# Kernel tuning notes

Hardware: AMD Instinct MI355X
Metric: run time of the kernel (lower is better)

Reference implementation:

```python
import jax, jax.numpy as jnp
import numpy as np

T = 4096
INPUT_SIZE = 64
DIMS = 64          # __init__ forces dimensions = input_size
RESERVOIR = 2048
OUTPUT_SIZE = 1
SPECTRAL_RADIUS = 0.95


def setup_inputs() -> dict:
    key = jax.random.key(0)
    k_x, k_c, k_in, k_res, k_w, k_b = jax.random.split(key, 6)
    X = jax.random.normal(k_x, (T, INPUT_SIZE, 1), dtype=jnp.float32)
    # conversion matrix: random then QR -> orthonormal columns
    C_raw = jax.random.uniform(k_c, (DIMS, INPUT_SIZE), dtype=jnp.float32)
    C, _ = jnp.linalg.qr(C_raw)
    # ESN weights. W_res entries ~ N(0, 1/RESERVOIR): circular-law spectral
    # radius ~= 1, scaled to the target spectral radius.
    W_in = jax.random.uniform(k_in, (RESERVOIR, DIMS), dtype=jnp.float32, minval=-1.0, maxval=1.0)
    W_res = jax.random.normal(k_res, (RESERVOIR, RESERVOIR), dtype=jnp.float32) * (SPECTRAL_RADIUS / np.sqrt(RESERVOIR))
    dense_W = jax.random.normal(k_w, (OUTPUT_SIZE, RESERVOIR + DIMS), dtype=jnp.float32) * 0.02
    dense_b = jnp.zeros((OUTPUT_SIZE,), dtype=jnp.float32)
    return {"X": X, "C": C, "W_in": W_in, "W_res": W_res,
            "dense_W": dense_W, "dense_b": dense_b}


def reference(X, C, W_in, W_res, dense_W, dense_b):
    # project all inputs up front: u_t = C @ x_t   -> (T, DIMS)
    U = jnp.einsum('di,tio->tdo', C, X)[..., 0]
    # sequential reservoir recurrence: h_t = tanh(W_in u_t + W_res h_{t-1})
    def step(h, u):
        h_new = jnp.tanh(W_in @ u + W_res @ h)
        return h_new, h_new
    h0 = jnp.zeros((W_res.shape[0],), dtype=X.dtype)
    _, H = jax.lax.scan(step, h0, U)            # (T, RESERVOIR)
    # ESN forward returns vstack(u, h); dense1 reads its transpose
    feats = jnp.concatenate([U, H], axis=1)     # (T, DIMS + RESERVOIR)
    y = feats @ dense_W.T + dense_b             # (T, OUTPUT_SIZE)
    # torch: stack of (1, OUTPUT) rows -> (T,1,OUT), permute(0,2,1) -> (T,OUT,1)
    return y[:, :, None]
```

## Files before the change

### kernel.cpp

```cpp
#include <hip/hip_runtime.h>

#define TT 4096

typedef __attribute__((ext_vector_type(2))) unsigned int u2v;
typedef __attribute__((ext_vector_type(4))) unsigned int u4v;
typedef __attribute__((ext_vector_type(2))) __fp16 f16x2;
typedef __attribute__((ext_vector_type(2))) _Float16 F16x2;
union HU { unsigned int u; f16x2 hf; F16x2 hF; };


__global__ void esn_prep(const float* __restrict__ C,
                         const float* __restrict__ Win,
                         const float* __restrict__ dW,
                         float* __restrict__ M,
                         float* __restrict__ wtil) {
  __shared__ float s[64];
  const int b = blockIdx.x, i = threadIdx.x;
  if (b < 2048) {
    s[i] = Win[b * 64 + i];
    __syncthreads();
    float acc = 0.f;
#pragma unroll 16
    for (int d = 0; d < 64; ++d) acc += s[d] * C[d * 64 + i];
    M[b * 64 + i] = acc;
  } else {
    s[i] = dW[i];
    __syncthreads();
    float acc = 0.f;
    for (int d = 0; d < 64; ++d) acc += s[d] * C[d * 64 + i];
    wtil[i] = acc;
  }
}

__device__ __forceinline__ float fast_tanh(float x) {
  const float e = __builtin_amdgcn_exp2f(x * 2.8853900817779268f);
  return 1.0f - 2.0f * __builtin_amdgcn_rcpf(e + 1.0f);
}

__device__ __forceinline__ float fdot2f(const HU a, const HU b, float c) {
#if __has_builtin(__builtin_amdgcn_fdot2)
  return __builtin_amdgcn_fdot2(a.hF, b.hF, c, false);
#else
  return c + (float)a.hf.x * (float)b.hf.x + (float)a.hf.y * (float)b.hf.y;
#endif
}

__global__ __launch_bounds__(1024) void esn_recur(
    const float* __restrict__ X, const float* __restrict__ M,
    const float* __restrict__ W, const float* __restrict__ dW,
    unsigned int* __restrict__ hpub, float* __restrict__ yp) {
  __shared__ unsigned int shh[1024];
  __shared__ unsigned int pub[16];
  __shared__ float psm[16];
  const int tid = threadIdx.x;
  const int lane = tid & 63;
  const int wave = tid >> 6;
  const int b = blockIdx.x;
  const int r0 = b * 32 + wave * 2;
  const float m0 = M[r0 * 64 + lane];
  const float m1 = M[(r0 + 1) * 64 + lane];
  const float dw0 = dW[64 + r0];
  const float dw1 = dW[64 + r0 + 1];
  u4v wA[4], wB[4];
#pragma unroll
  for (int j = 0; j < 4; ++j) {
    const float* p0 = W + (size_t)r0 * 2048 + 512 * j + 8 * lane;
    const float* p1 = p0 + 2048;
    const float4 a = *(const float4*)p0;
    const float4 c = *(const float4*)(p0 + 4);
    const float4 d = *(const float4*)p1;
    const float4 e = *(const float4*)(p1 + 4);
    HU t0, t1, t2, t3;
    t0.hf = __builtin_amdgcn_cvt_pkrtz(a.x, a.y);
    t1.hf = __builtin_amdgcn_cvt_pkrtz(a.z, a.w);
    t2.hf = __builtin_amdgcn_cvt_pkrtz(c.x, c.y);
    t3.hf = __builtin_amdgcn_cvt_pkrtz(c.z, c.w);
    wA[j][0] = t0.u; wA[j][1] = t1.u; wA[j][2] = t2.u; wA[j][3] = t3.u;
    t0.hf = __builtin_amdgcn_cvt_pkrtz(d.x, d.y);
    t1.hf = __builtin_amdgcn_cvt_pkrtz(d.z, d.w);
    t2.hf = __builtin_amdgcn_cvt_pkrtz(e.x, e.y);
    t3.hf = __builtin_amdgcn_cvt_pkrtz(e.z, e.w);
    wB[j][0] = t0.u; wB[j][1] = t1.u; wB[j][2] = t2.u; wB[j][3] = t3.u;
  }
  shh[tid] = 0u;
  __syncthreads();

  float xv = X[lane];

  for (int t = 0; t < TT; ++t) {
    float a0 = m0 * xv, a1 = m1 * xv;
#pragma unroll
    for (int j = 0; j < 4; ++j) {
      const u4v hv = *(const u4v*)(shh + 4 * lane + 256 * j);
#pragma unroll
      for (int k = 0; k < 4; ++k) {
        HU ha, wa, wb;
        ha.u = hv[k]; wa.u = wA[j][k]; wb.u = wB[j][k];
        a0 = fdot2f(wa, ha, a0);
        a1 = fdot2f(wb, ha, a1);
      }
    }
#pragma unroll
    for (int off = 32; off; off >>= 1) {
      a0 += __shfl_xor(a0, off, 64);
      a1 += __shfl_xor(a1, off, 64);
    }
    const int tn = (t + 1 < TT) ? t + 1 : t;
    const float xnext = X[tn * 64 + lane];
    if (lane == 0) {
      const float h0 = fast_tanh(a0);
      const float h1 = fast_tanh(a1);
      HU pk; pk.hf = __builtin_amdgcn_cvt_pkrtz(h0, h1);
      pub[wave] = pk.u;
      psm[wave] = dw0 * h0 + dw1 * h1;
    }
    __syncthreads();
    const unsigned tg = (unsigned)t + 1u;
    if (wave == 0) {
      if (t + 1 < TT) {
        unsigned int* slot = hpub + ((t & 1) << 11);
        if (tid < 16) {
          u2v pv; pv.x = pub[tid]; pv.y = tg;
          asm volatile("global_store_dwordx2 %0, %1, off sc0 sc1"
                       :: "v"(slot + 2 * (16 * b + tid)), "v"(pv) : "memory");
        }
        const unsigned int* b0 = slot + 2 * lane;
        const unsigned int* b1 = b0 + 1024;
        u2v q0, q1, q2, q3, q4, q5, q6, q7, q8, q9, qa, qb, qc, qd, qe, qf;
        for (;;) {
          asm volatile(
              "global_load_dwordx2 %0, %16, off sc0 sc1\n\t"
              "global_load_dwordx2 %1, %16, off offset:512 sc0 sc1\n\t"
              "global_load_dwordx2 %2, %16, off offset:1024 sc0 sc1\n\t"
              "global_load_dwordx2 %3, %16, off offset:1536 sc0 sc1\n\t"
              "global_load_dwordx2 %4, %16, off offset:2048 sc0 sc1\n\t"
              "global_load_dwordx2 %5, %16, off offset:2560 sc0 sc1\n\t"
              "global_load_dwordx2 %6, %16, off offset:3072 sc0 sc1\n\t"
              "global_load_dwordx2 %7, %16, off offset:3584 sc0 sc1\n\t"
              "global_load_dwordx2 %8, %17, off sc0 sc1\n\t"
              "global_load_dwordx2 %9, %17, off offset:512 sc0 sc1\n\t"
              "global_load_dwordx2 %10, %17, off offset:1024 sc0 sc1\n\t"
              "global_load_dwordx2 %11, %17, off offset:1536 sc0 sc1\n\t"
              "global_load_dwordx2 %12, %17, off offset:2048 sc0 sc1\n\t"
              "global_load_dwordx2 %13, %17, off offset:2560 sc0 sc1\n\t"
              "global_load_dwordx2 %14, %17, off offset:3072 sc0 sc1\n\t"
              "global_load_dwordx2 %15, %17, off offset:3584 sc0 sc1\n\t"
              "s_waitcnt vmcnt(0)"
              : "=&v"(q0), "=&v"(q1), "=&v"(q2), "=&v"(q3),
                "=&v"(q4), "=&v"(q5), "=&v"(q6), "=&v"(q7),
                "=&v"(q8), "=&v"(q9), "=&v"(qa), "=&v"(qb),
                "=&v"(qc), "=&v"(qd), "=&v"(qe), "=&v"(qf)
              : "v"(b0), "v"(b1)
              : "memory");
          bool ok = (q0.y == tg) && (q1.y == tg) && (q2.y == tg) &&
                    (q3.y == tg) && (q4.y == tg) && (q5.y == tg) &&
                    (q6.y == tg) && (q7.y == tg) && (q8.y == tg) &&
                    (q9.y == tg) && (qa.y == tg) && (qb.y == tg) &&
                    (qc.y == tg) && (qd.y == tg) && (qe.y == tg) &&
                    (qf.y == tg);
          if (__all(ok)) break;
        }
        shh[lane] = q0.x;          shh[64 + lane] = q1.x;
        shh[128 + lane] = q2.x;    shh[192 + lane] = q3.x;
        shh[256 + lane] = q4.x;    shh[320 + lane] = q5.x;
        shh[384 + lane] = q6.x;    shh[448 + lane] = q7.x;
        shh[512 + lane] = q8.x;    shh[576 + lane] = q9.x;
        shh[640 + lane] = qa.x;    shh[704 + lane] = qb.x;
        shh[768 + lane] = qc.x;    shh[832 + lane] = qd.x;
        shh[896 + lane] = qe.x;    shh[960 + lane] = qf.x;
      }
    } else if (tid == 64) {
      float s = 0.f;
#pragma unroll
      for (int wv = 0; wv < 16; ++wv) s += psm[wv];
      yp[t * 64 + b] = s;
    }
    __syncthreads();
    xv = xnext;
  }
}

__global__ void esn_out(const float* __restrict__ X,
                        const float* __restrict__ wtil,
                        const float* __restrict__ yp,
                        const float* __restrict__ bptr,
                        float* __restrict__ out) {
  const int tid = threadIdx.x;
  const int lane = tid & 63;
  const int wave = tid >> 6;
  const int t = blockIdx.x * 4 + wave;
  float v = wtil[lane] * X[t * 64 + lane] + yp[t * 64 + lane];
#pragma unroll
  for (int off = 32; off; off >>= 1) v += __shfl_xor(v, off, 64);
  if (lane == 0) out[t] = v + bptr[0];
}

extern "C" void kernel_launch(void* const* d_in, const int* in_sizes, int n_in,
                              void* d_out, int out_size, void* d_ws, size_t ws_size,
                              hipStream_t stream) {
  const float* X   = (const float*)d_in[0];
  const float* C   = (const float*)d_in[1];
  const float* Win = (const float*)d_in[2];
  const float* W   = (const float*)d_in[3];
  const float* dW  = (const float*)d_in[4];
  const float* db  = (const float*)d_in[5];
  float* ws   = (float*)d_ws;
  float* M    = ws;
  float* wtil = ws + 131072;
  float* yp   = ws + 131200;
  unsigned int* hpub = (unsigned int*)(ws + 393344);

  esn_prep<<<2049, 64, 0, stream>>>(C, Win, dW, M, wtil);

  void* args[] = {(void*)&X, (void*)&M, (void*)&W, (void*)&dW,
                  (void*)&hpub, (void*)&yp};
  (void)hipLaunchCooperativeKernel(reinterpret_cast<void*>(&esn_recur), dim3(64),
                                   dim3(1024), args, 0, stream);

  esn_out<<<1024, 256, 0, stream>>>(X, wtil, yp, db, (float*)d_out);
}
```

Before: 9.629 ms.

## Publish reservoir state per wave via atomics and double-buffer polling loads

Each wave's lane 0 now publishes its packed fp16 state with a relaxed agent-scope atomic exchange directly, instead of staging through shared memory and a block barrier before wave 0 stores. Wave 0 polls with two interleaved batches of flag loads so one batch is always in flight while the other is checked. The __syncthreads calls become raw s_barrier with an lgkmcnt wait. The aim is to shorten the per-timestep cross-block exchange latency, at the cost of more polling traffic and hand-managed waitcnt ordering that could be fragile.

```diff
diff --git a/kernel.cpp b/kernel.cpp
--- a/kernel.cpp
+++ b/kernel.cpp
@@ -45,12 +45,64 @@
 #endif
 }
 
+#define BARK() asm volatile("s_waitcnt lgkmcnt(0)\n\ts_barrier" ::: "memory")
+
+#define PISSUE(P, WAITSTR)                                              \
+  asm volatile(                                                         \
+      "global_load_dwordx2 %0, %16, off sc0 sc1\n\t"                    \
+      "global_load_dwordx2 %1, %16, off offset:512 sc0 sc1\n\t"         \
+      "global_load_dwordx2 %2, %16, off offset:1024 sc0 sc1\n\t"        \
+      "global_load_dwordx2 %3, %16, off offset:1536 sc0 sc1\n\t"        \
+      "global_load_dwordx2 %4, %16, off offset:2048 sc0 sc1\n\t"        \
+      "global_load_dwordx2 %5, %16, off offset:2560 sc0 sc1\n\t"        \
+      "global_load_dwordx2 %6, %16, off offset:3072 sc0 sc1\n\t"        \
+      "global_load_dwordx2 %7, %16, off offset:3584 sc0 sc1\n\t"        \
+      "global_load_dwordx2 %8, %17, off sc0 sc1\n\t"                    \
+      "global_load_dwordx2 %9, %17, off offset:512 sc0 sc1\n\t"         \
+      "global_load_dwordx2 %10, %17, off offset:1024 sc0 sc1\n\t"       \
+      "global_load_dwordx2 %11, %17, off offset:1536 sc0 sc1\n\t"       \
+      "global_load_dwordx2 %12, %17, off offset:2048 sc0 sc1\n\t"       \
+      "global_load_dwordx2 %13, %17, off offset:2560 sc0 sc1\n\t"       \
+      "global_load_dwordx2 %14, %17, off offset:3072 sc0 sc1\n\t"       \
+      "global_load_dwordx2 %15, %17, off offset:3584 sc0 sc1" WAITSTR   \
+      : "=&v"(P##0), "=&v"(P##1), "=&v"(P##2), "=&v"(P##3),             \
+        "=&v"(P##4), "=&v"(P##5), "=&v"(P##6), "=&v"(P##7),             \
+        "=&v"(P##8), "=&v"(P##9), "=&v"(P##a), "=&v"(P##b),             \
+        "=&v"(P##c), "=&v"(P##d), "=&v"(P##e), "=&v"(P##f)              \
+      : "v"(b0), "v"(b1)                                                \
+      : "memory")
+
+#define REGBAR(P)                                                       \
+  asm volatile("" : "+v"(P##0), "+v"(P##1), "+v"(P##2), "+v"(P##3),     \
+                    "+v"(P##4), "+v"(P##5), "+v"(P##6), "+v"(P##7),     \
+                    "+v"(P##8), "+v"(P##9), "+v"(P##a), "+v"(P##b),     \
+                    "+v"(P##c), "+v"(P##d), "+v"(P##e), "+v"(P##f))
+
+#define CHK(P)                                                          \
+  __all(((P##0).y == tg) && ((P##1).y == tg) && ((P##2).y == tg) &&     \
+        ((P##3).y == tg) && ((P##4).y == tg) && ((P##5).y == tg) &&     \
+        ((P##6).y == tg) && ((P##7).y == tg) && ((P##8).y == tg) &&     \
+        ((P##9).y == tg) && ((P##a).y == tg) && ((P##b).y == tg) &&     \
+        ((P##c).y == tg) && ((P##d).y == tg) && ((P##e).y == tg) &&     \
+        ((P##f).y == tg))
+
+#define REPACK(P)                                                       \
+  do {                                                                  \
+    shh[lane] = (P##0).x;          shh[64 + lane] = (P##1).x;           \
+    shh[128 + lane] = (P##2).x;    shh[192 + lane] = (P##3).x;          \
+    shh[256 + lane] = (P##4).x;    shh[320 + lane] = (P##5).x;          \
+    shh[384 + lane] = (P##6).x;    shh[448 + lane] = (P##7).x;          \
+    shh[512 + lane] = (P##8).x;    shh[576 + lane] = (P##9).x;          \
+    shh[640 + lane] = (P##a).x;    shh[704 + lane] = (P##b).x;          \
+    shh[768 + lane] = (P##c).x;    shh[832 + lane] = (P##d).x;          \
+    shh[896 + lane] = (P##e).x;    shh[960 + lane] = (P##f).x;          \
+  } while (0)
+
 __global__ __launch_bounds__(1024) void esn_recur(
     const float* __restrict__ X, const float* __restrict__ M,
     const float* __restrict__ W, const float* __restrict__ dW,
     unsigned int* __restrict__ hpub, float* __restrict__ yp) {
   __shared__ unsigned int shh[1024];
-  __shared__ unsigned int pub[16];
   __shared__ float psm[16];
   const int tid = threadIdx.x;
   const int lane = tid & 63;
@@ -105,69 +157,47 @@
       a0 += __shfl_xor(a0, off, 64);
       a1 += __shfl_xor(a1, off, 64);
     }
+    const unsigned tg = (unsigned)t + 1u;
+    unsigned int* slot = hpub + ((t & 1) << 11);
     const int tn = (t + 1 < TT) ? t + 1 : t;
     const float xnext = X[tn * 64 + lane];
     if (lane == 0) {
       const float h0 = fast_tanh(a0);
       const float h1 = fast_tanh(a1);
       HU pk; pk.hf = __builtin_amdgcn_cvt_pkrtz(h0, h1);
-      pub[wave] = pk.u;
       psm[wave] = dw0 * h0 + dw1 * h1;
-    }
-    __syncthreads();
-    const unsigned tg = (unsigned)t + 1u;
+      if (t + 1 < TT) {
+        const unsigned long long pk64 =
+            ((unsigned long long)tg << 32) | (unsigned long long)pk.u;
+        (void)__hip_atomic_exchange(
+            (unsigned long long*)(slot + 2 * (16 * b + wave)), pk64,
+            __ATOMIC_RELAXED, __HIP_MEMORY_SCOPE_AGENT);
+      }
+    }
+    BARK();
     if (wave == 0) {
       if (t + 1 < TT) {
-        unsigned int* slot = hpub + ((t & 1) << 11);
-        if (tid < 16) {
-          u2v pv; pv.x = pub[tid]; pv.y = tg;
-          asm volatile("global_store_dwordx2 %0, %1, off sc0 sc1"
-                       :: "v"(slot + 2 * (16 * b + tid)), "v"(pv) : "memory");
-        }
         const unsigned int* b0 = slot + 2 * lane;
         const unsigned int* b1 = b0 + 1024;
-        u2v q0, q1, q2, q3, q4, q5, q6, q7, q8, q9, qa, qb, qc, qd, qe, qf;
-        for (;;) {
-          asm volatile(
-              "global_load_dwordx2 %0, %16, off sc0 sc1\n\t"
-              "global_load_dwordx2 %1, %16, off offset:512 sc0 sc1\n\t"
-              "global_load_dwordx2 %2, %16, off offset:1024 sc0 sc1\n\t"
-              "global_load_dwordx2 %3, %16, off offset:1536 sc0 sc1\n\t"
-              "global_load_dwordx2 %4, %16, off offset:2048 sc0 sc1\n\t"
-              "global_load_dwordx2 %5, %16, off offset:2560 sc0 sc1\n\t"
-              "global_load_dwordx2 %6, %16, off offset:3072 sc0 sc1\n\t"
-              "global_load_dwordx2 %7, %16, off offset:3584 sc0 sc1\n\t"
-              "global_load_dwordx2 %8, %17, off sc0 sc1\n\t"
-              "global_load_dwordx2 %9, %17, off offset:512 sc0 sc1\n\t"
-              "global_load_dwordx2 %10, %17, off offset:1024 sc0 sc1\n\t"
-              "global_load_dwordx2 %11, %17, off offset:1536 sc0 sc1\n\t"
-              "global_load_dwordx2 %12, %17, off offset:2048 sc0 sc1\n\t"
-              "global_load_dwordx2 %13, %17, off offset:2560 sc0 sc1\n\t"
-              "global_load_dwordx2 %14, %17, off offset:3072 sc0 sc1\n\t"
-              "global_load_dwordx2 %15, %17, off offset:3584 sc0 sc1\n\t"
-              "s_waitcnt vmcnt(0)"
-              : "=&v"(q0), "=&v"(q1), "=&v"(q2), "=&v"(q3),
-                "=&v"(q4), "=&v"(q5), "=&v"(q6), "=&v"(q7),
-                "=&v"(q8), "=&v"(q9), "=&v"(qa), "=&v"(qb),
-                "=&v"(qc), "=&v"(qd), "=&v"(qe), "=&v"(qf)
-              : "v"(b0), "v"(b1)
-              : "memory");
-          bool ok = (q0.y == tg) && (q1.y == tg) && (q2.y == tg) &&
-                    (q3.y == tg) && (q4.y == tg) && (q5.y == tg) &&
-                    (q6.y == tg) && (q7.y == tg) && (q8.y == tg) &&
-                    (q9.y == tg) && (qa.y == tg) && (qb.y == tg) &&
-                    (qc.y == tg) && (qd.y == tg) && (qe.y == tg) &&
-                    (qf.y == tg);
-          if (__all(ok)) break;
+        u2v A0, A1, A2, A3, A4, A5, A6, A7, A8, A9, Aa, Ab, Ac, Ad, Ae, Af;
+        u2v B0, B1, B2, B3, B4, B5, B6, B7, B8, B9, Ba, Bb, Bc, Bd, Be, Bf;
+        asm volatile("s_waitcnt vmcnt(1)" ::: "memory");
+        PISSUE(A, "");
+        PISSUE(B, "\n\ts_waitcnt vmcnt(16)");
+        REGBAR(A);
+        bool useB = false;
+        bool got = CHK(A);
+        if (!got) {
+          for (;;) {
+            PISSUE(A, "\n\ts_waitcnt vmcnt(16)");
+            REGBAR(B);
+            if (CHK(B)) { useB = true; break; }
+            PISSUE(B, "\n\ts_waitcnt vmcnt(16)");
+            REGBAR(A);
+            if (CHK(A)) { useB = false; break; }
+          }
         }
-        shh[lane] = q0.x;          shh[64 + lane] = q1.x;
-        shh[128 + lane] = q2.x;    shh[192 + lane] = q3.x;
-        shh[256 + lane] = q4.x;    shh[320 + lane] = q5.x;
-        shh[384 + lane] = q6.x;    shh[448 + lane] = q7.x;
-        shh[512 + lane] = q8.x;    shh[576 + lane] = q9.x;
-        shh[640 + lane] = qa.x;    shh[704 + lane] = qb.x;
-        shh[768 + lane] = qc.x;    shh[832 + lane] = qd.x;
-        shh[896 + lane] = qe.x;    shh[960 + lane] = qf.x;
+        if (useB) REPACK(B); else REPACK(A);
       }
     } else if (tid == 64) {
       float s = 0.f;
@@ -175,7 +205,7 @@
       for (int wv = 0; wv < 16; ++wv) s += psm[wv];
       yp[t * 64 + b] = s;
     }
-    __syncthreads();
+    BARK();
     xv = xnext;
   }
 }
```

Measured after the change: 12.11 ms. 25.8% more time.
